# Optimization experiments

Measured on AMD Instinct MI355X. Metric: run time of the kernel, lower is better.

Reference implementation:

```python
import jax, jax.numpy as jnp
import numpy as np

EPS = 1e-8

def setup_inputs() -> dict:
    key = jax.random.key(0)
    k1, k2 = jax.random.split(key)
    B, IN, OUT, G = 32768, 256, 256, 5
    x = jax.random.normal(k1, (B, IN), dtype=jnp.float32)
    grid = jnp.linspace(-1.0, 1.0, G).astype(jnp.float32)
    coef = jax.random.normal(k2, (OUT, IN, G), dtype=jnp.float32) * 0.1
    scale = jnp.ones((OUT, IN), dtype=jnp.float32)
    bias = jnp.zeros((OUT,), dtype=jnp.float32)
    return {"x": x, "grid": grid, "coef": coef, "scale": scale, "bias": bias}

def reference(x, grid, coef, scale, bias):
    # global min-max normalization to [-1, 1]
    xmin, xmax = x.min(), x.max()
    xn = 2.0 * (x - xmin) / (xmax - xmin + EPS) - 1.0
    # cubic bump B-spline-like basis: (batch, in, grid)
    dist = jnp.abs(xn[..., None] - grid)
    basis = jnp.where(dist < 1.0, 1.0 - dist ** 3, 0.0)
    basis = basis / (basis.sum(axis=-1, keepdims=True) + EPS)
    # fused contraction over (in, grid); equals ((basis*coef).sum(-1)*scale).sum(-1)
    w = coef * scale[..., None]          # (out, in, grid)
    out = jnp.einsum('big,oig->bo', basis, w) + bias
    return out
```

## Files before the change

### kernel.cpp

```cpp
#include <hip/hip_runtime.h>
#include <stdint.h>


#define B_SZ   32768
#define IN_SZ  256
#define OUT_SZ 256
#define EPSF   1e-8f
#define NMB    2048

typedef __bf16 bf16x8 __attribute__((ext_vector_type(8)));
typedef unsigned short ushort8 __attribute__((ext_vector_type(8)));
typedef float floatx16 __attribute__((ext_vector_type(16)));

union frag_u { uint4 u; bf16x8 v; };

#define PKHH 0x07060302u
#define PKLL 0x05040100u
#define PKHL 0x05040302u

__device__ __forceinline__ unsigned short f2bf(float f) {
  unsigned u = __float_as_uint(f);
  u += 0x7FFFu + ((u >> 16) & 1u);
  return (unsigned short)(u >> 16);
}


__global__ void __launch_bounds__(256) prep_kernel(const float* __restrict__ coef,
                                                   const float* __restrict__ scale,
                                                   const float* __restrict__ x,
                                                   unsigned short* __restrict__ wf,
                                                   float* __restrict__ part, int n4) {
  const int t = threadIdx.x;
  if (blockIdx.x < 160) {
    int b = blockIdx.x;
    int c = b / 10, r = b - c * 10;
    int kt = r >> 1, lh = r & 1;
    int o = t;
    const float* cp = coef + (size_t)o * 1280 + c * 80 + lh * 40 + kt * 8;
    const float* sp = scale + o * 256 + c * 16 + lh * 8;
    ushort8 v;
    #pragma unroll
    for (int j = 0; j < 8; ++j) {
      int il = (kt * 8 + j) / 5;
      v[j] = f2bf(cp[j] * sp[il]);
    }
    int seg = (c * 8 + (o >> 5)) * 5 + kt;
    *(ushort8*)(wf + (size_t)seg * 512 + (lh * 32 + (o & 31)) * 8) = v;
  } else {
    int mb = blockIdx.x - 160;
    const float4* x4 = (const float4*)x;
    int i = mb * 256 + t;
    float lmin = 1e30f, lmax = -1e30f;
    #pragma unroll
    for (int k = 0; k < 4; ++k) {
      float4 v = x4[i + k * (NMB * 256)];
      lmin = fminf(lmin, fminf(fminf(v.x, v.y), fminf(v.z, v.w)));
      lmax = fmaxf(lmax, fmaxf(fmaxf(v.x, v.y), fmaxf(v.z, v.w)));
    }
    #pragma unroll
    for (int off = 32; off >= 1; off >>= 1) {
      lmin = fminf(lmin, __shfl_down(lmin, off, 64));
      lmax = fmaxf(lmax, __shfl_down(lmax, off, 64));
    }
    __shared__ float smn[4], smx[4];
    if ((t & 63) == 0) { smn[t >> 6] = lmin; smx[t >> 6] = lmax; }
    __syncthreads();
    if (t == 0) {
      part[2 * mb]     = fminf(fminf(smn[0], smn[1]), fminf(smn[2], smn[3]));
      part[2 * mb + 1] = fmaxf(fmaxf(smx[0], smx[1]), fmaxf(smx[2], smx[3]));
    }
  }
}

struct quint { unsigned u0, u1, u2; };

__device__ __forceinline__ quint quintet(float xval, float scA, float scB) {
  float xn = fmaf(xval, scA, scB);
  float d0 = xn + 1.0f, d1 = xn + 0.5f, d3 = xn - 0.5f, d4 = xn - 1.0f;
  float b0 = fmaxf(fmaf(d0 * d0, -fabsf(d0), 1.0f), 0.0f);
  float b1 = fmaxf(fmaf(d1 * d1, -fabsf(d1), 1.0f), 0.0f);
  float b2 = fmaxf(fmaf(xn * xn, -fabsf(xn), 1.0f), 0.0f);
  float b3 = fmaxf(fmaf(d3 * d3, -fabsf(d3), 1.0f), 0.0f);
  float b4 = fmaxf(fmaf(d4 * d4, -fabsf(d4), 1.0f), 0.0f);
  float sum = ((b0 + b1) + (b2 + b3)) + b4;
  float inv = __builtin_amdgcn_rcpf(sum);
  b0 *= inv; b1 *= inv; b2 *= inv; b3 *= inv; b4 *= inv;
  quint q;
  q.u0 = __builtin_amdgcn_perm(__float_as_uint(b1), __float_as_uint(b0), PKHH);
  q.u1 = __builtin_amdgcn_perm(__float_as_uint(b3), __float_as_uint(b2), PKHH);
  q.u2 = __float_as_uint(b4) >> 16;
  return q;
}

__global__ void __launch_bounds__(256, 2) kan_gemm(
    const float* __restrict__ x,
    const unsigned short* __restrict__ wf,
    const float* __restrict__ bias,
    const float* __restrict__ part,
    float* __restrict__ out)
{
  __shared__ __align__(16) unsigned short Bb[2][10240];
  __shared__ float2 red[4];

  const int t = threadIdx.x;
  const int lane = t & 63;
  const int wm = t >> 6;
  const int l31 = lane & 31, lh = lane >> 5;
  const int bRow = blockIdx.x * 128;
  const int bCol = blockIdx.y * 128;
  const int row = bRow + wm * 32 + l31;

  auto stage = [&](int c, int buf) {
    #pragma unroll
    for (int r = 0; r < 5; ++r) {
      const unsigned short* src = wf +
          ((size_t)((c * 8 + blockIdx.y * 4 + wm) * 5 + r)) * 512 + (size_t)lane * 8;
      __builtin_amdgcn_global_load_lds(
          (const __attribute__((address_space(1))) unsigned int*)src,
          (__attribute__((address_space(3))) unsigned int*)(&Bb[buf][(r * 4 + wm) * 512 + lane * 8]),
          16, 0, 0);
    }
  };

  const float* xrow = x + (size_t)row * IN_SZ;

  stage(0, 0);
  float4 xq[4], xqn[4];
  #pragma unroll
  for (int g = 0; g < 4; ++g) xq[g] = *(const float4*)(xrow + g * 4);

  float mn = 1e30f, mx = -1e30f;
  const float2* part2 = (const float2*)part;
  #pragma unroll
  for (int k = 0; k < NMB / 256; ++k) {
    float2 p = part2[k * 256 + t];
    mn = fminf(mn, p.x); mx = fmaxf(mx, p.y);
  }
  #pragma unroll
  for (int off = 32; off >= 1; off >>= 1) {
    mn = fminf(mn, __shfl_down(mn, off, 64));
    mx = fmaxf(mx, __shfl_down(mx, off, 64));
  }
  if (lane == 0) red[wm] = make_float2(mn, mx);
  __syncthreads();
  mn = fminf(fminf(red[0].x, red[1].x), fminf(red[2].x, red[3].x));
  mx = fmaxf(fmaxf(red[0].y, red[1].y), fmaxf(red[2].y, red[3].y));
  const float scA = 2.0f / (mx - mn + EPSF);
  const float scB = -mn * scA - 1.0f;

  floatx16 acc[4] = {};
  bf16x8 br[2][4];

  auto ldsB = [&](int kt, int buf, bf16x8* dst) {
    #pragma unroll
    for (int q = 0; q < 4; ++q)
      dst[q] = *(const bf16x8*)(&Bb[buf][(kt * 4 + q) * 512 + lane * 8]);
  };

  for (int c = 0; c < 16; ++c) {
    const int buf = c & 1;

    __syncthreads();

    if (c < 15) {
      stage(c + 1, buf ^ 1);
      #pragma unroll
      for (int g = 0; g < 4; ++g)
        xqn[g] = *(const float4*)(xrow + (c + 1) * 16 + g * 4);
    }

    ldsB(0, buf, br[0]);

    float4 xa = lh ? xq[2] : xq[0];
    float4 xb = lh ? xq[3] : xq[1];
    quint q0 = quintet(xa.x, scA, scB), q1 = quintet(xa.y, scA, scB);
    quint q2 = quintet(xa.z, scA, scB), q3 = quintet(xa.w, scA, scB);
    quint q4 = quintet(xb.x, scA, scB), q5 = quintet(xb.y, scA, scB);
    quint q6 = quintet(xb.z, scA, scB), q7 = quintet(xb.w, scA, scB);

    frag_u a;
    bf16x8* B;

    ldsB(1, buf, br[1]);
    a.u.x = q0.u0; a.u.y = q0.u1;
    a.u.z = __builtin_amdgcn_perm(q1.u0, q0.u2, PKLL);
    a.u.w = __builtin_amdgcn_perm(q1.u1, q1.u0, PKHL);
    B = br[0];
    #pragma unroll
    for (int ni = 0; ni < 4; ++ni)
      acc[ni] = __builtin_amdgcn_mfma_f32_32x32x16_bf16(a.v, B[ni], acc[ni], 0, 0, 0);

    ldsB(2, buf, br[0]);
    a.u.x = __builtin_amdgcn_perm(q1.u2, q1.u1, PKHL);
    a.u.y = q2.u0; a.u.z = q2.u1;
    a.u.w = __builtin_amdgcn_perm(q3.u0, q2.u2, PKLL);
    B = br[1];
    #pragma unroll
    for (int ni = 0; ni < 4; ++ni)
      acc[ni] = __builtin_amdgcn_mfma_f32_32x32x16_bf16(a.v, B[ni], acc[ni], 0, 0, 0);

    ldsB(3, buf, br[1]);
    a.u.x = __builtin_amdgcn_perm(q3.u1, q3.u0, PKHL);
    a.u.y = __builtin_amdgcn_perm(q3.u2, q3.u1, PKHL);
    a.u.z = q4.u0; a.u.w = q4.u1;
    B = br[0];
    #pragma unroll
    for (int ni = 0; ni < 4; ++ni)
      acc[ni] = __builtin_amdgcn_mfma_f32_32x32x16_bf16(a.v, B[ni], acc[ni], 0, 0, 0);

    ldsB(4, buf, br[0]);
    a.u.x = __builtin_amdgcn_perm(q5.u0, q4.u2, PKLL);
    a.u.y = __builtin_amdgcn_perm(q5.u1, q5.u0, PKHL);
    a.u.z = __builtin_amdgcn_perm(q5.u2, q5.u1, PKHL);
    a.u.w = q6.u0;
    B = br[1];
    #pragma unroll
    for (int ni = 0; ni < 4; ++ni)
      acc[ni] = __builtin_amdgcn_mfma_f32_32x32x16_bf16(a.v, B[ni], acc[ni], 0, 0, 0);

    a.u.x = q6.u1;
    a.u.y = __builtin_amdgcn_perm(q7.u0, q6.u2, PKLL);
    a.u.z = __builtin_amdgcn_perm(q7.u1, q7.u0, PKHL);
    a.u.w = __builtin_amdgcn_perm(q7.u2, q7.u1, PKHL);
    B = br[0];
    #pragma unroll
    for (int ni = 0; ni < 4; ++ni)
      acc[ni] = __builtin_amdgcn_mfma_f32_32x32x16_bf16(a.v, B[ni], acc[ni], 0, 0, 0);

    if (c < 15) {
      #pragma unroll
      for (int g = 0; g < 4; ++g) xq[g] = xqn[g];
    }
  }

  #pragma unroll
  for (int ni = 0; ni < 4; ++ni) {
    int o = bCol + ni * 32 + l31;
    float bs = bias[o];
    int rb = bRow + wm * 32 + 4 * lh;
    #pragma unroll
    for (int reg = 0; reg < 16; ++reg) {
      int r = rb + (reg & 3) + 8 * (reg >> 2);
      out[(size_t)r * OUT_SZ + o] = acc[ni][reg] + bs;
    }
  }
}

extern "C" void kernel_launch(void* const* d_in, const int* in_sizes, int n_in,
                              void* d_out, int out_size, void* d_ws, size_t ws_size,
                              hipStream_t stream) {
  const float* x     = (const float*)d_in[0];
  const float* coef  = (const float*)d_in[2];
  const float* scale = (const float*)d_in[3];
  const float* bias  = (const float*)d_in[4];
  float* out = (float*)d_out;

  size_t need = 16384 + (size_t)640 * 1024;
  if (ws_size < need) return;

  float* part = (float*)d_ws;
  unsigned short* wf = (unsigned short*)((char*)d_ws + 16384);

  prep_kernel<<<160 + NMB, 256, 0, stream>>>(coef, scale, x, wf, part,
                                             (B_SZ * IN_SZ) / 4);
  dim3 g(B_SZ / 128, OUT_SZ / 128);
  kan_gemm<<<g, 256, 0, stream>>>(x, wf, bias, part, out);
}
```

Measured before the change: 123.4 us.

## Load B fragments directly from global into registers, drop LDS staging

Removes the shared-memory double buffer and per-chunk __syncthreads, and instead loads each wave's B fragments straight from global memory into a 4-deep register ring two phases ahead. The K loop is restructured into macro-unrolled groups with ping-pong x prefetch, and s_setprio is raised around the MFMA bursts. The goal is to cut LDS traffic and barrier stalls, at the cost of more VGPRs and reliance on L2/cache hits for repeated B reads across blocks. The workspace size is enlarged, probably to keep the prefetch past the last chunk in bounds.

```diff
diff --git a/kernel.cpp b/kernel.cpp
--- a/kernel.cpp
+++ b/kernel.cpp
@@ -92,6 +92,76 @@
   return q;
 }
 
+template<int R>
+__device__ __forceinline__ bf16x8 assembleA(const quint* q) {
+  frag_u a;
+  if constexpr (R == 0) {
+    a.u.x = q[0].u0;
+    a.u.y = q[0].u1;
+    a.u.z = __builtin_amdgcn_perm(q[1].u0, q[0].u2, PKLL);
+    a.u.w = __builtin_amdgcn_perm(q[1].u1, q[1].u0, PKHL);
+  } else if constexpr (R == 1) {
+    a.u.x = __builtin_amdgcn_perm(q[1].u2, q[1].u1, PKHL);
+    a.u.y = q[2].u0;
+    a.u.z = q[2].u1;
+    a.u.w = __builtin_amdgcn_perm(q[3].u0, q[2].u2, PKLL);
+  } else if constexpr (R == 2) {
+    a.u.x = __builtin_amdgcn_perm(q[3].u1, q[3].u0, PKHL);
+    a.u.y = __builtin_amdgcn_perm(q[3].u2, q[3].u1, PKHL);
+    a.u.z = q[4].u0;
+    a.u.w = q[4].u1;
+  } else if constexpr (R == 3) {
+    a.u.x = __builtin_amdgcn_perm(q[5].u0, q[4].u2, PKLL);
+    a.u.y = __builtin_amdgcn_perm(q[5].u1, q[5].u0, PKHL);
+    a.u.z = __builtin_amdgcn_perm(q[5].u2, q[5].u1, PKHL);
+    a.u.w = q[6].u0;
+  } else {
+    a.u.x = q[6].u1;
+    a.u.y = __builtin_amdgcn_perm(q[7].u0, q[6].u2, PKLL);
+    a.u.z = __builtin_amdgcn_perm(q[7].u1, q[7].u0, PKHL);
+    a.u.w = __builtin_amdgcn_perm(q[7].u2, q[7].u1, PKHL);
+  }
+  return a.v;
+}
+
+#define PHASE(J, R)                                                          \
+  {                                                                          \
+    constexpr int cc2 = ((J) + 2) / 5, rr2 = ((J) + 2) % 5;                  \
+    const int c2 = o4 + cc2;                                                 \
+    Bs[((J) + 2) & 3][0] = wfl[((c2 * 8 + 0) * 5 + rr2) * 64];               \
+    Bs[((J) + 2) & 3][1] = wfl[((c2 * 8 + 1) * 5 + rr2) * 64];               \
+    Bs[((J) + 2) & 3][2] = wfl[((c2 * 8 + 2) * 5 + rr2) * 64];               \
+    Bs[((J) + 2) & 3][3] = wfl[((c2 * 8 + 3) * 5 + rr2) * 64];               \
+    bf16x8 a = assembleA<R>(qq);                                             \
+    frag_u b0, b1, b2, b3;                                                   \
+    b0.u = Bs[(J) & 3][0]; b1.u = Bs[(J) & 3][1];                            \
+    b2.u = Bs[(J) & 3][2]; b3.u = Bs[(J) & 3][3];                            \
+    __builtin_amdgcn_s_setprio(1);                                           \
+    acc[0] = __builtin_amdgcn_mfma_f32_32x32x16_bf16(a, b0.v, acc[0], 0,0,0);\
+    acc[1] = __builtin_amdgcn_mfma_f32_32x32x16_bf16(a, b1.v, acc[1], 0,0,0);\
+    acc[2] = __builtin_amdgcn_mfma_f32_32x32x16_bf16(a, b2.v, acc[2], 0,0,0);\
+    acc[3] = __builtin_amdgcn_mfma_f32_32x32x16_bf16(a, b3.v, acc[3], 0,0,0);\
+    __builtin_amdgcn_s_setprio(0);                                           \
+  }
+
+#define GROUP(GG, XC0, XC1, XN0, XN1, PREF)                                  \
+  {                                                                          \
+    if (PREF) {                                                              \
+      XN0 = *(const float4*)(xrowh + (o4 + (GG) + 1) * 16);                  \
+      XN1 = *(const float4*)(xrowh + (o4 + (GG) + 1) * 16 + 4);              \
+    }                                                                        \
+    quint qq[8];                                                             \
+    qq[0] = quintet(XC0.x, scA, scB); qq[1] = quintet(XC0.y, scA, scB);      \
+    qq[2] = quintet(XC0.z, scA, scB); qq[3] = quintet(XC0.w, scA, scB);      \
+    qq[4] = quintet(XC1.x, scA, scB); qq[5] = quintet(XC1.y, scA, scB);      \
+    qq[6] = quintet(XC1.z, scA, scB); qq[7] = quintet(XC1.w, scA, scB);      \
+    PHASE((GG) * 5 + 0, 0)                                                   \
+    PHASE((GG) * 5 + 1, 1)                                                   \
+    PHASE((GG) * 5 + 2, 2)                                                   \
+    PHASE((GG) * 5 + 3, 3)                                                   \
+    PHASE((GG) * 5 + 4, 4)                                                   \
+  }
+
 __global__ void __launch_bounds__(256, 2) kan_gemm(
     const float* __restrict__ x,
     const unsigned short* __restrict__ wf,
@@ -99,7 +169,6 @@
     const float* __restrict__ part,
     float* __restrict__ out)
 {
-  __shared__ __align__(16) unsigned short Bb[2][10240];
   __shared__ float2 red[4];
 
   const int t = threadIdx.x;
@@ -110,24 +179,22 @@
   const int bCol = blockIdx.y * 128;
   const int row = bRow + wm * 32 + l31;
 
-  auto stage = [&](int c, int buf) {
-    #pragma unroll
-    for (int r = 0; r < 5; ++r) {
-      const unsigned short* src = wf +
-          ((size_t)((c * 8 + blockIdx.y * 4 + wm) * 5 + r)) * 512 + (size_t)lane * 8;
-      __builtin_amdgcn_global_load_lds(
-          (const __attribute__((address_space(1))) unsigned int*)src,
-          (__attribute__((address_space(3))) unsigned int*)(&Bb[buf][(r * 4 + wm) * 512 + lane * 8]),
-          16, 0, 0);
-    }
-  };
-
-  const float* xrow = x + (size_t)row * IN_SZ;
-
-  stage(0, 0);
-  float4 xq[4], xqn[4];
-  #pragma unroll
-  for (int g = 0; g < 4; ++g) xq[g] = *(const float4*)(xrow + g * 4);
+  const uint4* wfl = (const uint4*)wf + (size_t)blockIdx.y * 1280 + lane;
+
+  const float* xrowh = x + (size_t)row * IN_SZ + lh * 8;
+
+  uint4 Bs[4][4];
+  Bs[0][0] = wfl[((0 * 8 + 0) * 5 + 0) * 64];
+  Bs[0][1] = wfl[((0 * 8 + 1) * 5 + 0) * 64];
+  Bs[0][2] = wfl[((0 * 8 + 2) * 5 + 0) * 64];
+  Bs[0][3] = wfl[((0 * 8 + 3) * 5 + 0) * 64];
+  Bs[1][0] = wfl[((0 * 8 + 0) * 5 + 1) * 64];
+  Bs[1][1] = wfl[((0 * 8 + 1) * 5 + 1) * 64];
+  Bs[1][2] = wfl[((0 * 8 + 2) * 5 + 1) * 64];
+  Bs[1][3] = wfl[((0 * 8 + 3) * 5 + 1) * 64];
+  float4 xA0 = *(const float4*)(xrowh);
+  float4 xA1 = *(const float4*)(xrowh + 4);
+  float4 xB0, xB1;
 
   float mn = 1e30f, mx = -1e30f;
   const float2* part2 = (const float2*)part;
@@ -149,88 +216,12 @@
   const float scB = -mn * scA - 1.0f;
 
   floatx16 acc[4] = {};
-  bf16x8 br[2][4];
-
-  auto ldsB = [&](int kt, int buf, bf16x8* dst) {
-    #pragma unroll
-    for (int q = 0; q < 4; ++q)
-      dst[q] = *(const bf16x8*)(&Bb[buf][(kt * 4 + q) * 512 + lane * 8]);
-  };
-
-  for (int c = 0; c < 16; ++c) {
-    const int buf = c & 1;
-
-    __syncthreads();
-
-    if (c < 15) {
-      stage(c + 1, buf ^ 1);
-      #pragma unroll
-      for (int g = 0; g < 4; ++g)
-        xqn[g] = *(const float4*)(xrow + (c + 1) * 16 + g * 4);
-    }
-
-    ldsB(0, buf, br[0]);
-
-    float4 xa = lh ? xq[2] : xq[0];
-    float4 xb = lh ? xq[3] : xq[1];
-    quint q0 = quintet(xa.x, scA, scB), q1 = quintet(xa.y, scA, scB);
-    quint q2 = quintet(xa.z, scA, scB), q3 = quintet(xa.w, scA, scB);
-    quint q4 = quintet(xb.x, scA, scB), q5 = quintet(xb.y, scA, scB);
-    quint q6 = quintet(xb.z, scA, scB), q7 = quintet(xb.w, scA, scB);
-
-    frag_u a;
-    bf16x8* B;
-
-    ldsB(1, buf, br[1]);
-    a.u.x = q0.u0; a.u.y = q0.u1;
-    a.u.z = __builtin_amdgcn_perm(q1.u0, q0.u2, PKLL);
-    a.u.w = __builtin_amdgcn_perm(q1.u1, q1.u0, PKHL);
-    B = br[0];
-    #pragma unroll
-    for (int ni = 0; ni < 4; ++ni)
-      acc[ni] = __builtin_amdgcn_mfma_f32_32x32x16_bf16(a.v, B[ni], acc[ni], 0, 0, 0);
-
-    ldsB(2, buf, br[0]);
-    a.u.x = __builtin_amdgcn_perm(q1.u2, q1.u1, PKHL);
-    a.u.y = q2.u0; a.u.z = q2.u1;
-    a.u.w = __builtin_amdgcn_perm(q3.u0, q2.u2, PKLL);
-    B = br[1];
-    #pragma unroll
-    for (int ni = 0; ni < 4; ++ni)
-      acc[ni] = __builtin_amdgcn_mfma_f32_32x32x16_bf16(a.v, B[ni], acc[ni], 0, 0, 0);
-
-    ldsB(3, buf, br[1]);
-    a.u.x = __builtin_amdgcn_perm(q3.u1, q3.u0, PKHL);
-    a.u.y = __builtin_amdgcn_perm(q3.u2, q3.u1, PKHL);
-    a.u.z = q4.u0; a.u.w = q4.u1;
-    B = br[0];
-    #pragma unroll
-    for (int ni = 0; ni < 4; ++ni)
-      acc[ni] = __builtin_amdgcn_mfma_f32_32x32x16_bf16(a.v, B[ni], acc[ni], 0, 0, 0);
-
-    ldsB(4, buf, br[0]);
-    a.u.x = __builtin_amdgcn_perm(q5.u0, q4.u2, PKLL);
-    a.u.y = __builtin_amdgcn_perm(q5.u1, q5.u0, PKHL);
-    a.u.z = __builtin_amdgcn_perm(q5.u2, q5.u1, PKHL);
-    a.u.w = q6.u0;
-    B = br[1];
-    #pragma unroll
-    for (int ni = 0; ni < 4; ++ni)
-      acc[ni] = __builtin_amdgcn_mfma_f32_32x32x16_bf16(a.v, B[ni], acc[ni], 0, 0, 0);
-
-    a.u.x = q6.u1;
-    a.u.y = __builtin_amdgcn_perm(q7.u0, q6.u2, PKLL);
-    a.u.z = __builtin_amdgcn_perm(q7.u1, q7.u0, PKHL);
-    a.u.w = __builtin_amdgcn_perm(q7.u2, q7.u1, PKHL);
-    B = br[0];
-    #pragma unroll
-    for (int ni = 0; ni < 4; ++ni)
-      acc[ni] = __builtin_amdgcn_mfma_f32_32x32x16_bf16(a.v, B[ni], acc[ni], 0, 0, 0);
-
-    if (c < 15) {
-      #pragma unroll
-      for (int g = 0; g < 4; ++g) xq[g] = xqn[g];
-    }
+
+  for (int o = 0, o4 = 0; o < 4; ++o, o4 += 4) {
+    GROUP(0, xA0, xA1, xB0, xB1, true)
+    GROUP(1, xB0, xB1, xA0, xA1, true)
+    GROUP(2, xA0, xA1, xB0, xB1, true)
+    GROUP(3, xB0, xB1, xA0, xA1, (o4 < 12))
   }
 
   #pragma unroll
@@ -255,7 +246,7 @@
   const float* bias  = (const float*)d_in[4];
   float* out = (float*)d_out;
 
-  size_t need = 16384 + (size_t)640 * 1024;
+  size_t need = 16384 + (size_t)704 * 1024;
   if (ws_size < need) return;
 
   float* part = (float*)d_ws;
```

New measurement: 119.9 us. 1.03x faster.
